# Kernel optimization log

Measured on AMD Instinct MI355X. Metric: run time of the kernel, lower is better.

Reference implementation:

```python
import jax, jax.numpy as jnp
import numpy as np

B, S, E, H, VP, L, T = 256, 256, 1024, 1024, 8, 64, 16


def setup_inputs() -> dict:
    key = jax.random.key(0)
    ks = jax.random.split(key, 10)
    image = jax.random.normal(ks[0], (B, S, E), jnp.float32)
    view_position = jax.random.uniform(ks[1], (B, VP), jnp.float32)
    label = (jax.random.uniform(ks[2], (B, T + 1, L)) > 0.5).astype(jnp.float32)
    # lengths sorted descending (length_sorted_rnn decorator), max forced to T+1
    length = jnp.sort(jax.random.randint(ks[3], (B,), 2, T + 2))[::-1]
    length = length.at[0].set(T + 1)
    def lin(k, out_d, in_d):
        return jax.random.normal(k, (out_d, in_d), jnp.float32) * (1.0 / np.sqrt(in_d)).astype(np.float32)
    IN = E + VP + 1 + L  # 1097: lstm_sizes = [embedding, view_position, 1, label]
    FC_OUT = L + H + 1 + 1  # 1090: fc_sizes = [label, hidden, 1, 1]
    return {
        'image': image, 'view_position': view_position, 'label': label, 'length': length,
        'W_h': lin(ks[4], H, E), 'b_h': jnp.zeros((H,), jnp.float32),
        'W_m': lin(ks[5], H, E), 'b_m': jnp.zeros((H,), jnp.float32),
        'W_ih': lin(ks[6], 4 * H, IN), 'W_hh': lin(ks[7], 4 * H, H),
        'b_ih': jnp.zeros((4 * H,), jnp.float32), 'b_hh': jnp.zeros((4 * H,), jnp.float32),
        'W_fc': lin(ks[8], FC_OUT, H), 'b_fc': jnp.zeros((FC_OUT,), jnp.float32),
    }


def reference(image, view_position, label, length, W_h, b_h, W_m, b_m,
              W_ih, W_hh, b_ih, b_hh, W_fc, b_fc):
    # Dropout is identity (inference). image: (B,S,E)
    image_mean = image.mean(axis=1)                      # (B,E)
    h0 = jnp.tanh(image_mean @ W_h.T + b_h)              # (B,H)
    m0 = jnp.tanh(image_mean @ W_m.T + b_m)              # (B,H)
    n_steps = label.shape[1] - 1
    bsz = image_mean.shape[0]

    def step(carry, inp):
        h, m = carry
        lab_t, t = inp
        begin = jnp.where(t == 0, 1.0, 0.0) * jnp.ones((bsz, 1), image_mean.dtype)
        x = jnp.concatenate([image_mean, view_position, begin, lab_t], axis=1)  # (B, 1097)
        gates = x @ W_ih.T + b_ih + h @ W_hh.T + b_hh    # (B, 4H)
        i, f, g, o = jnp.split(gates, 4, axis=1)
        m2 = jax.nn.sigmoid(f) * m + jax.nn.sigmoid(i) * jnp.tanh(g)
        h2 = jax.nn.sigmoid(o) * jnp.tanh(m2)
        out = h2 @ W_fc.T + b_fc                         # (B, L+H+2)
        topic = jax.nn.relu(out[:, L:L + H])
        stop = jax.nn.sigmoid(out[:, L + H:L + H + 1])
        temp = jnp.exp(out[:, L + H + 1:])
        return (h2, m2), jnp.concatenate([topic, stop, temp], axis=1)

    labels_tm = jnp.swapaxes(label[:, :n_steps], 0, 1)   # (T,B,L) time-major
    _, outs = jax.lax.scan(step, (h0, m0), (labels_tm, jnp.arange(n_steps)))
    # pad_sequence semantics: entries with t >= length-1 are zero padding
    mask = (jnp.arange(n_steps)[:, None] < (length - 1)[None, :]).astype(outs.dtype)
    return outs * mask[:, :, None]                       # (T, B, H+2) = [topic|stop|temp]
```

## Files before the change

kernel.cpp:

```cpp
#include <hip/hip_runtime.h>
#include <stdint.h>

typedef unsigned short u16;
typedef __attribute__((ext_vector_type(8))) short v8s;
typedef __attribute__((ext_vector_type(4))) float v4f;

__device__ __forceinline__ u16 f2bf(float f) {
  uint32_t x = __float_as_uint(f);
  return (u16)((x + 0x7fffu + ((x >> 16) & 1u)) >> 16);
}
__device__ __forceinline__ float bf2f(u16 u) {
  return __uint_as_float(((uint32_t)u) << 16);
}
__device__ __forceinline__ float sigf(float x) { return 1.f / (1.f + __expf(-x)); }

__device__ __forceinline__ v4f mfma16(v8s a, v8s b, v4f c) {
  return __builtin_amdgcn_mfma_f32_16x16x32_bf16(a, b, c, 0, 0, 0);
}

__device__ __forceinline__ void gll16(const u16* src, u16* ldsdst) {
  __builtin_amdgcn_global_load_lds(
      reinterpret_cast<__attribute__((address_space(1))) uint32_t*>(
          reinterpret_cast<uintptr_t>(src)),
      reinterpret_cast<__attribute__((address_space(3))) uint32_t*>(
          reinterpret_cast<uintptr_t>(ldsdst)),
      16, 0, 0);
}

__device__ __forceinline__ size_t fpoff(int row, int k, int KT) {
  return ((size_t)(((row >> 4) * KT + (k >> 6)) * 2 + ((k >> 5) & 1)) * 64 +
          ((k >> 3) & 3) * 16 + (row & 15)) * 8 + (k & 7);
}

__device__ __forceinline__ void load8(const float* p, float* f) {
  float4 a = *(const float4*)p;
  float4 b = *(const float4*)(p + 4);
  f[0]=a.x; f[1]=a.y; f[2]=a.z; f[3]=a.w; f[4]=b.x; f[5]=b.y; f[6]=b.z; f[7]=b.w;
}
__device__ __forceinline__ void store8bf(u16* dst, const float* f) {
  u16 t[8];
#pragma unroll
  for (int i = 0; i < 8; ++i) t[i] = f2bf(f[i]);
  *(v8s*)dst = *(const v8s*)t;
}

__global__ __launch_bounds__(256) void k_convert_mean(
    const float* __restrict__ Wh, const float* __restrict__ Wm,
    const float* __restrict__ Wih, const float* __restrict__ Whh,
    const float* __restrict__ Wfc, const float* __restrict__ label,
    const float* __restrict__ image,
    u16* __restrict__ wcomb, u16* __restrict__ whhb, u16* __restrict__ wfcb,
    u16* __restrict__ wlabb, u16* __restrict__ labb,
    float4* __restrict__ pacc, unsigned* __restrict__ ctr) {
  const int bid = blockIdx.x, tid = threadIdx.x;
  if (bid >= 8000) {
    ctr[(bid - 8000) * 256 + tid] = 0u;
    return;
  }
  if (bid >= 5952) {
    int bi = bid - 5952;
    int b = bi >> 3, oct = bi & 7;
    const float4* src =
        (const float4*)image + (size_t)b * 65536 + (size_t)oct * 32 * 256 + tid;
    float4 s = make_float4(0.f, 0.f, 0.f, 0.f);
#pragma unroll 8
    for (int ss = 0; ss < 32; ++ss) {
      float4 v = src[(size_t)ss * 256];
      s.x += v.x; s.y += v.y; s.z += v.z; s.w += v.w;
    }
    pacc[(size_t)bi * 256 + tid] = s;
    return;
  }
  int64_t u = (int64_t)bid * 256 + tid;
  float f[8];
  if (u < 786432) {
    int lu = (int)u;
    int r15 = lu & 15, q = (lu >> 4) & 3, s = (lu >> 6) & 1, tile = lu >> 7;
    int tk = tile & 15, tr = tile >> 4;
    int row = tr * 16 + r15, k = tk * 64 + s * 32 + q * 8;
    if (row < 1024) load8(Wh + (size_t)row * 1024 + k, f);
    else if (row < 2048) load8(Wm + (size_t)(row - 1024) * 1024 + k, f);
    else {
      const float* p = Wih + (size_t)(row - 2048) * 1097 + k;
#pragma unroll
      for (int i = 0; i < 8; ++i) f[i] = p[i];
    }
    store8bf(wcomb + (size_t)lu * 8, f);
  } else if (u < 1310720) {
    int lu = (int)(u - 786432);
    int r15 = lu & 15, q = (lu >> 4) & 3, s = (lu >> 6) & 1, tile = lu >> 7;
    int tk = tile & 15, tr = tile >> 4;
    int row = tr * 16 + r15, k = tk * 64 + s * 32 + q * 8;
    load8(Whh + (size_t)row * 1024 + k, f);
    store8bf(whhb + (size_t)lu * 8, f);
  } else if (u < 1458176) {
    int lu = (int)(u - 1310720);
    int r15 = lu & 15, q = (lu >> 4) & 3, s = (lu >> 6) & 1, tile = lu >> 7;
    int tk = tile & 15, tr = tile >> 4;
    int row = tr * 16 + r15, k = tk * 64 + s * 32 + q * 8;
    if (row < 1090) load8(Wfc + (size_t)row * 1024 + k, f);
    else {
#pragma unroll
      for (int i = 0; i < 8; ++i) f[i] = 0.f;
    }
    store8bf(wfcb + (size_t)lu * 8, f);
  } else if (u < 1490944) {
    int lu = (int)(u - 1458176);
    int r15 = lu & 15, q = (lu >> 4) & 3, s = (lu >> 6) & 1, tile = lu >> 7;
    int row = tile * 16 + r15, k = s * 32 + q * 8;
    const float* p = Wih + (size_t)row * 1097 + 1033 + k;
#pragma unroll
    for (int i = 0; i < 8; ++i) f[i] = p[i];
    store8bf(wlabb + (size_t)lu * 8, f);
  } else {
    int lu = (int)(u - 1490944);
    int r15 = lu & 15, q = (lu >> 4) & 3, s = (lu >> 6) & 1, tile = lu >> 7;
    int row = tile * 16 + r15, k = s * 32 + q * 8;
    int t = row >> 8, b = row & 255;
    load8(label + ((size_t)b * 17 + t) * 64 + k, f);
    store8bf(labb + (size_t)lu * 8, f);
  }
}

__global__ __launch_bounds__(256) void k_mean2(const float4* __restrict__ pacc,
                                               u16* __restrict__ meanbf) {
  int b = blockIdx.x, tid = threadIdx.x;
  float4 s = make_float4(0.f, 0.f, 0.f, 0.f);
#pragma unroll
  for (int q = 0; q < 8; ++q) {
    float4 v = pacc[((size_t)b * 8 + q) * 256 + tid];
    s.x += v.x; s.y += v.y; s.z += v.z; s.w += v.w;
  }
  const float inv = 1.f / 256.f;
  int k = tid * 4;
  ushort4 o;
  o.x = f2bf(s.x * inv); o.y = f2bf(s.y * inv);
  o.z = f2bf(s.z * inv); o.w = f2bf(s.w * inv);
  *(ushort4*)&meanbf[fpoff(b, k, 16)] = o;
}

__global__ __launch_bounds__(256) void k_gemm_init(
    const u16* __restrict__ meanbf, const u16* __restrict__ wcomb,
    const float* __restrict__ bh, const float* __restrict__ bm,
    const float* __restrict__ bih, const float* __restrict__ bhh,
    const float* __restrict__ vp, const float* __restrict__ Wih,
    u16* __restrict__ hbuf, float* __restrict__ mbuf, float* __restrict__ basebuf) {
  __shared__ alignas(16) u16 lA[4 * 1024];
  __shared__ alignas(16) u16 lB[4 * 1024];
  const int tid = threadIdx.x, lane = tid & 63, wid = tid >> 6;
  const int bm0 = (blockIdx.x & 3) * 64;
  const int bn0 = (blockIdx.x >> 2) * 64;
  const int wr = wid >> 1, wc = wid & 1;
  v4f acc[2][2];
#pragma unroll
  for (int i = 0; i < 2; ++i)
#pragma unroll
    for (int j = 0; j < 2; ++j) acc[i][j] = (v4f){0.f, 0.f, 0.f, 0.f};

  for (int kt = 0; kt < 16; ++kt) {
    const u16* asrc = meanbf + ((size_t)((bm0 >> 4) + wid) * 16 + kt) * 1024 + lane * 8;
    gll16(asrc, lA + wid * 1024);
    gll16(asrc + 512, lA + wid * 1024 + 512);
    const u16* bsrc = wcomb + ((size_t)((bn0 >> 4) + wid) * 16 + kt) * 1024 + lane * 8;
    gll16(bsrc, lB + wid * 1024);
    gll16(bsrc + 512, lB + wid * 1024 + 512);
    __syncthreads();
#pragma unroll
    for (int s = 0; s < 2; ++s) {
      v8s a0 = *(const v8s*)&lA[(size_t)(wr * 2) * 1024 + s * 512 + lane * 8];
      v8s a1 = *(const v8s*)&lA[(size_t)(wr * 2 + 1) * 1024 + s * 512 + lane * 8];
      v8s b0 = *(const v8s*)&lB[(size_t)(wc * 2) * 1024 + s * 512 + lane * 8];
      v8s b1 = *(const v8s*)&lB[(size_t)(wc * 2 + 1) * 1024 + s * 512 + lane * 8];
      acc[0][0] = mfma16(a0, b0, acc[0][0]);
      acc[0][1] = mfma16(a0, b1, acc[0][1]);
      acc[1][0] = mfma16(a1, b0, acc[1][0]);
      acc[1][1] = mfma16(a1, b1, acc[1][1]);
    }
    __syncthreads();
  }
#pragma unroll
  for (int fm = 0; fm < 2; ++fm)
#pragma unroll
    for (int fn = 0; fn < 2; ++fn)
#pragma unroll
      for (int rg = 0; rg < 4; ++rg) {
        int row = bm0 + wr * 32 + fm * 16 + ((lane >> 4) << 2) + rg;
        int col = bn0 + wc * 32 + fn * 16 + (lane & 15);
        float v = acc[fm][fn][rg];
        if (col < 1024) {
          hbuf[fpoff(row, col, 16)] = f2bf(tanhf(v + bh[col]));
        } else if (col < 2048) {
          int nn = col - 1024;
          mbuf[(size_t)row * 1024 + nn] = tanhf(v + bm[nn]);
        } else {
          int j = col - 2048;
          float sv = v + bih[j] + bhh[j];
#pragma unroll
          for (int q = 0; q < 8; ++q)
            sv += vp[row * 8 + q] * Wih[(size_t)j * 1097 + 1024 + q];
          basebuf[(size_t)row * 4096 + j] = sv;
        }
      }
}

__global__ __launch_bounds__(256) void k_basefull(
    const u16* __restrict__ labb, const u16* __restrict__ wlabb,
    const float* __restrict__ basebuf, const float* __restrict__ Wih,
    u16* __restrict__ bfull) {
  __shared__ alignas(16) u16 lA[4 * 1024];
  __shared__ alignas(16) u16 lB[4 * 1024];
  const int tid = threadIdx.x, lane = tid & 63, wid = tid >> 6;
  const int bm0 = (blockIdx.x & 63) * 64;
  const int bn0 = (blockIdx.x >> 6) * 64;
  const int wr = wid >> 1, wc = wid & 1;
  v4f acc[2][2];
#pragma unroll
  for (int i = 0; i < 2; ++i)
#pragma unroll
    for (int j = 0; j < 2; ++j) acc[i][j] = (v4f){0.f, 0.f, 0.f, 0.f};

  const u16* asrc = labb + (size_t)((bm0 >> 4) + wid) * 1024 + lane * 8;
  gll16(asrc, lA + wid * 1024);
  gll16(asrc + 512, lA + wid * 1024 + 512);
  const u16* bsrc = wlabb + (size_t)((bn0 >> 4) + wid) * 1024 + lane * 8;
  gll16(bsrc, lB + wid * 1024);
  gll16(bsrc + 512, lB + wid * 1024 + 512);
  __syncthreads();
#pragma unroll
  for (int s = 0; s < 2; ++s) {
    v8s a0 = *(const v8s*)&lA[(size_t)(wr * 2) * 1024 + s * 512 + lane * 8];
    v8s a1 = *(const v8s*)&lA[(size_t)(wr * 2 + 1) * 1024 + s * 512 + lane * 8];
    v8s b0 = *(const v8s*)&lB[(size_t)(wc * 2) * 1024 + s * 512 + lane * 8];
    v8s b1 = *(const v8s*)&lB[(size_t)(wc * 2 + 1) * 1024 + s * 512 + lane * 8];
    acc[0][0] = mfma16(a0, b0, acc[0][0]);
    acc[0][1] = mfma16(a0, b1, acc[0][1]);
    acc[1][0] = mfma16(a1, b0, acc[1][0]);
    acc[1][1] = mfma16(a1, b1, acc[1][1]);
  }
#pragma unroll
  for (int fm = 0; fm < 2; ++fm)
#pragma unroll
    for (int fn = 0; fn < 2; ++fn)
#pragma unroll
      for (int rg = 0; rg < 4; ++rg) {
        int r = bm0 + wr * 32 + fm * 16 + ((lane >> 4) << 2) + rg;
        int j = bn0 + wc * 32 + fn * 16 + (lane & 15);
        int t = r >> 8, b = r & 255;
        float v = acc[fm][fn][rg] + basebuf[(size_t)b * 4096 + j];
        if (t == 0) v += Wih[(size_t)j * 1097 + 1032];
        bfull[(size_t)r * 4096 + j] = f2bf(v);
      }
}

__global__ __launch_bounds__(256, 1) void k_steps(
    const u16* __restrict__ whhb, const u16* __restrict__ bfull,
    const float* __restrict__ mbuf, u16* __restrict__ hbuf,
    unsigned* __restrict__ ctr) {
  __shared__ alignas(16) u16 lA[64 * 512];
  __shared__ alignas(16) u16 lBias[8 * 512];
  __shared__ alignas(16) float lact[4][32 * 33];
  const int tid = threadIdx.x, lane = tid & 63, wid = tid >> 6;
  const int blk = blockIdx.x;
  const int n0idx = (blk & 7) * 4 + (blk >> 6);
  const int n0 = n0idx * 32;
  const int grp = (blk >> 3) & 7;
  const int b0 = grp * 32;
  const int atr = b0 >> 4;

  const int tr0 = wid * 64 + (n0 >> 4);
  v8s breg[16][2][2];
#pragma unroll
  for (int kt = 0; kt < 16; ++kt)
#pragma unroll
    for (int s = 0; s < 2; ++s)
#pragma unroll
      for (int j = 0; j < 2; ++j)
        breg[kt][s][j] =
            *(const v8s*)&whhb[((size_t)(tr0 + j) * 16 + kt) * 1024 + s * 512 + lane * 8];

  const int rowm = tid >> 3;
  const int nql = (tid & 7) * 4;
  const int b = b0 + rowm;
  const int n = n0 + nql;
  float4 mreg = *(const float4*)&mbuf[(size_t)b * 1024 + n];

  for (int t = 0; t < 16; ++t) {
    if (t > 0) {
      const unsigned* f = &ctr[((t - 1) * 8 + grp) * 32];
      for (int it = 0; it < (1 << 18); ++it) {
        unsigned v = __hip_atomic_load(&f[lane & 31], __ATOMIC_RELAXED,
                                       __HIP_MEMORY_SCOPE_AGENT);
        if (__ballot(v == 0u) == 0ull) break;
        __builtin_amdgcn_s_sleep(1);
      }
    }
    const u16* hsrc = hbuf + (size_t)t * 262144;
    __builtin_amdgcn_sched_barrier(0);
#pragma unroll
    for (int j = 0; j < 8; ++j) {
      const int hc = wid * 8 + j;
      const int i = hc >> 4, kt = (hc >> 1) & 7, s = hc & 1;
      gll16(hsrc + ((size_t)(atr + i) * 16 + kt) * 1024 + s * 512 + lane * 8,
            lA + (i * 32 + kt * 2 + s) * 512);
    }
    __builtin_amdgcn_sched_barrier(0);
#pragma unroll
    for (int j = 0; j < 8; ++j) {
      const int hc = wid * 8 + j;
      const int i = hc >> 4, kt = ((hc >> 1) & 7) + 8, s = hc & 1;
      gll16(hsrc + ((size_t)(atr + i) * 16 + kt) * 1024 + s * 512 + lane * 8,
            lA + (i * 32 + kt * 2 + s) * 512);
    }
    __builtin_amdgcn_sched_barrier(0);
#pragma unroll
    for (int c2 = 0; c2 < 2; ++c2) {
      const u16* bsrc = bfull + (size_t)t * 1048576 +
                        (size_t)(b0 + c2 * 16 + (lane >> 2)) * 4096 +
                        wid * 1024 + n0 + (lane & 3) * 8;
      gll16(bsrc, lBias + (wid * 2 + c2) * 512);
    }
    __builtin_amdgcn_sched_barrier(0);
    asm volatile("s_waitcnt vmcnt(10)" ::: "memory");
    __builtin_amdgcn_sched_barrier(0);
    __builtin_amdgcn_s_barrier();
    __builtin_amdgcn_sched_barrier(0);

    v4f acc[2][2];
#pragma unroll
    for (int i = 0; i < 2; ++i)
#pragma unroll
      for (int j = 0; j < 2; ++j) acc[i][j] = (v4f){0.f, 0.f, 0.f, 0.f};
#pragma unroll
    for (int kt = 0; kt < 8; ++kt)
#pragma unroll
      for (int s = 0; s < 2; ++s) {
        v8s a0 = *(const v8s*)&lA[(size_t)((0 * 16 + kt) * 2 + s) * 512 + lane * 8];
        v8s a1 = *(const v8s*)&lA[(size_t)((1 * 16 + kt) * 2 + s) * 512 + lane * 8];
        acc[0][0] = mfma16(a0, breg[kt][s][0], acc[0][0]);
        acc[0][1] = mfma16(a0, breg[kt][s][1], acc[0][1]);
        acc[1][0] = mfma16(a1, breg[kt][s][0], acc[1][0]);
        acc[1][1] = mfma16(a1, breg[kt][s][1], acc[1][1]);
      }

    __builtin_amdgcn_sched_barrier(0);
    asm volatile("s_waitcnt vmcnt(2)" ::: "memory");
    __builtin_amdgcn_sched_barrier(0);
    __builtin_amdgcn_s_barrier();
    __builtin_amdgcn_sched_barrier(0);
#pragma unroll
    for (int kt = 8; kt < 16; ++kt)
#pragma unroll
      for (int s = 0; s < 2; ++s) {
        v8s a0 = *(const v8s*)&lA[(size_t)((0 * 16 + kt) * 2 + s) * 512 + lane * 8];
        v8s a1 = *(const v8s*)&lA[(size_t)((1 * 16 + kt) * 2 + s) * 512 + lane * 8];
        acc[0][0] = mfma16(a0, breg[kt][s][0], acc[0][0]);
        acc[0][1] = mfma16(a0, breg[kt][s][1], acc[0][1]);
        acc[1][0] = mfma16(a1, breg[kt][s][0], acc[1][0]);
        acc[1][1] = mfma16(a1, breg[kt][s][1], acc[1][1]);
      }

#pragma unroll
    for (int fm = 0; fm < 2; ++fm)
#pragma unroll
      for (int fn = 0; fn < 2; ++fn)
#pragma unroll
        for (int rg = 0; rg < 4; ++rg) {
          int rr = fm * 16 + ((lane >> 4) << 2) + rg;
          int cc = fn * 16 + (lane & 15);
          lact[wid][rr * 33 + cc] = acc[fm][fn][rg];
        }
    __syncthreads();

    const int bofs = ((rowm & 15) * 4 + (nql >> 3)) * 8 + (nql & 7);
    const int bch = (rowm >> 4) * 512;
    float m2a[4];
    u16 h2a[4];
#pragma unroll
    for (int q = 0; q < 4; ++q) {
      float gi = lact[0][rowm * 33 + nql + q] + bf2f(lBias[0 * 1024 + bch + bofs + q]);
      float gf = lact[1][rowm * 33 + nql + q] + bf2f(lBias[1 * 1024 + bch + bofs + q]);
      float gg = lact[2][rowm * 33 + nql + q] + bf2f(lBias[2 * 1024 + bch + bofs + q]);
      float go = lact[3][rowm * 33 + nql + q] + bf2f(lBias[3 * 1024 + bch + bofs + q]);
      float mov = ((const float*)&mreg)[q];
      float m2 = sigf(gf) * mov + sigf(gi) * tanhf(gg);
      float h2 = sigf(go) * tanhf(m2);
      m2a[q] = m2;
      h2a[q] = f2bf(h2);
    }
    mreg = make_float4(m2a[0], m2a[1], m2a[2], m2a[3]);
    ushort4 ho;
    ho.x = h2a[0]; ho.y = h2a[1]; ho.z = h2a[2]; ho.w = h2a[3];
    unsigned long long hv;
    __builtin_memcpy(&hv, &ho, 8);
    __hip_atomic_store(
        reinterpret_cast<unsigned long long*>(
            &hbuf[(size_t)(t + 1) * 262144 + fpoff(b, n, 16)]),
        hv, __ATOMIC_RELAXED, __HIP_MEMORY_SCOPE_AGENT);

    if (t < 15) {
      __syncthreads();
      if (tid == 0)
        __hip_atomic_store(&ctr[(t * 8 + grp) * 32 + n0idx], 1u,
                           __ATOMIC_RELAXED, __HIP_MEMORY_SCOPE_AGENT);
    }
  }
}

__global__ __launch_bounds__(256) void k_fc(
    const u16* __restrict__ hall, const u16* __restrict__ wfcb,
    const float* __restrict__ bfc, const int* __restrict__ length,
    float* __restrict__ out) {
  __shared__ alignas(16) u16 lA[4 * 1024];
  __shared__ alignas(16) u16 lB[4 * 1024];
  const int tid = threadIdx.x, lane = tid & 63, wid = tid >> 6;
  const int bm0 = (int)(blockIdx.x % 64) * 64;
  const int bn0 = (int)(blockIdx.x / 64) * 64;
  const int wr = wid >> 1, wc = wid & 1;
  v4f acc[2][2];
#pragma unroll
  for (int i = 0; i < 2; ++i)
#pragma unroll
    for (int j = 0; j < 2; ++j) acc[i][j] = (v4f){0.f, 0.f, 0.f, 0.f};

  for (int kt = 0; kt < 16; ++kt) {
    const u16* asrc = hall + ((size_t)((bm0 >> 4) + wid) * 16 + kt) * 1024 + lane * 8;
    gll16(asrc, lA + wid * 1024);
    gll16(asrc + 512, lA + wid * 1024 + 512);
    const u16* bsrc = wfcb + ((size_t)((bn0 >> 4) + wid) * 16 + kt) * 1024 + lane * 8;
    gll16(bsrc, lB + wid * 1024);
    gll16(bsrc + 512, lB + wid * 1024 + 512);
    __syncthreads();
#pragma unroll
    for (int s = 0; s < 2; ++s) {
      v8s a0 = *(const v8s*)&lA[(size_t)(wr * 2) * 1024 + s * 512 + lane * 8];
      v8s a1 = *(const v8s*)&lA[(size_t)(wr * 2 + 1) * 1024 + s * 512 + lane * 8];
      v8s b0 = *(const v8s*)&lB[(size_t)(wc * 2) * 1024 + s * 512 + lane * 8];
      v8s b1 = *(const v8s*)&lB[(size_t)(wc * 2 + 1) * 1024 + s * 512 + lane * 8];
      acc[0][0] = mfma16(a0, b0, acc[0][0]);
      acc[0][1] = mfma16(a0, b1, acc[0][1]);
      acc[1][0] = mfma16(a1, b0, acc[1][0]);
      acc[1][1] = mfma16(a1, b1, acc[1][1]);
    }
    __syncthreads();
  }
#pragma unroll
  for (int fm = 0; fm < 2; ++fm)
#pragma unroll
    for (int fn = 0; fn < 2; ++fn)
#pragma unroll
      for (int rg = 0; rg < 4; ++rg) {
        int r = bm0 + wr * 32 + fm * 16 + ((lane >> 4) << 2) + rg;
        int j = bn0 + wc * 32 + fn * 16 + (lane & 15);
        if (j < 64 || j >= 1090) continue;
        int t = r >> 8, b = r & 255;
        float v = acc[fm][fn][rg] + bfc[j];
        int c;
        if (j < 1088) { c = j - 64; v = fmaxf(v, 0.f); }
        else if (j == 1088) { c = 1024; v = 1.f / (1.f + expf(-v)); }
        else { c = 1025; v = expf(v); }
        if (t >= length[b] - 1) v = 0.f;
        out[((size_t)t * 256 + b) * 1026 + c] = v;
      }
}

extern "C" void kernel_launch(void* const* d_in, const int* in_sizes, int n_in,
                              void* d_out, int out_size, void* d_ws, size_t ws_size,
                              hipStream_t stream) {
  (void)in_sizes; (void)n_in; (void)out_size; (void)ws_size;
  const float* image  = (const float*)d_in[0];
  const float* vp     = (const float*)d_in[1];
  const float* label  = (const float*)d_in[2];
  const int*   length = (const int*)d_in[3];
  const float* Wh  = (const float*)d_in[4];
  const float* bh  = (const float*)d_in[5];
  const float* Wm  = (const float*)d_in[6];
  const float* bm  = (const float*)d_in[7];
  const float* Wih = (const float*)d_in[8];
  const float* Whh = (const float*)d_in[9];
  const float* bih = (const float*)d_in[10];
  const float* bhh = (const float*)d_in[11];
  const float* Wfc = (const float*)d_in[12];
  const float* bfc = (const float*)d_in[13];
  float* out = (float*)d_out;
  char* ws = (char*)d_ws;

  size_t off = 0;
  u16* wcomb  = (u16*)(ws + off); off += (size_t)6144 * 1024 * 2;
  u16* whhb   = (u16*)(ws + off); off += (size_t)4096 * 1024 * 2;
  u16* wfcb   = (u16*)(ws + off); off += (size_t)1152 * 1024 * 2;
  u16* wlabb  = (u16*)(ws + off); off += (size_t)4096 * 64 * 2;
  u16* labb   = (u16*)(ws + off); off += (size_t)4096 * 64 * 2;
  u16* meanbf = (u16*)(ws + off); off += (size_t)256 * 1024 * 2;
  u16* hbuf   = (u16*)(ws + off); off += (size_t)17 * 256 * 1024 * 2;
  float* mbuf    = (float*)(ws + off); off += (size_t)256 * 1024 * 4;
  float* basebuf = (float*)(ws + off); off += (size_t)256 * 4096 * 4;
  u16* bfull  = (u16*)(ws + off); off += (size_t)16 * 256 * 4096 * 2;
  unsigned* ctr = (unsigned*)(ws + off); off += 4096 * 4;
  float4* pacc = (float4*)bfull;

  k_convert_mean<<<8016, 256, 0, stream>>>(Wh, Wm, Wih, Whh, Wfc, label, image,
                                           wcomb, whhb, wfcb, wlabb, labb, pacc, ctr);
  k_mean2<<<256, 256, 0, stream>>>(pacc, meanbf);
  k_gemm_init<<<384, 256, 0, stream>>>(meanbf, wcomb, bh, bm, bih, bhh, vp, Wih,
                                       hbuf, mbuf, basebuf);
  k_basefull<<<4096, 256, 0, stream>>>(labb, wlabb, basebuf, Wih, bfull);
  k_steps<<<256, 256, 0, stream>>>(whhb, bfull, mbuf, hbuf, ctr);
  k_fc<<<1152, 256, 0, stream>>>(hbuf + (size_t)256 * 1024, wfcb, bfc, length, out);
}
```

Before: 225.6 us.

## Fuse label-projection GEMM into recurrent step kernel, drop bfull precompute

Removes the separate k_basefull kernel, which materialised a 16x256x4096 bf16 bias tensor. The recurrent kernel now loads the label tiles into LDS once and keeps the label weights and base biases in registers. Each step adds the label contribution with four extra MFMAs per wave. This saves one launch and a large global write and read, but adds LDS use (64 KB more), register pressure in a kernel limited to one block per CU, and compute on the serial critical path.

```diff
diff --git a/kernel.cpp b/kernel.cpp
--- a/kernel.cpp
+++ b/kernel.cpp
@@ -203,61 +203,13 @@
       }
 }
 
-__global__ __launch_bounds__(256) void k_basefull(
-    const u16* __restrict__ labb, const u16* __restrict__ wlabb,
-    const float* __restrict__ basebuf, const float* __restrict__ Wih,
-    u16* __restrict__ bfull) {
-  __shared__ alignas(16) u16 lA[4 * 1024];
-  __shared__ alignas(16) u16 lB[4 * 1024];
-  const int tid = threadIdx.x, lane = tid & 63, wid = tid >> 6;
-  const int bm0 = (blockIdx.x & 63) * 64;
-  const int bn0 = (blockIdx.x >> 6) * 64;
-  const int wr = wid >> 1, wc = wid & 1;
-  v4f acc[2][2];
-#pragma unroll
-  for (int i = 0; i < 2; ++i)
-#pragma unroll
-    for (int j = 0; j < 2; ++j) acc[i][j] = (v4f){0.f, 0.f, 0.f, 0.f};
-
-  const u16* asrc = labb + (size_t)((bm0 >> 4) + wid) * 1024 + lane * 8;
-  gll16(asrc, lA + wid * 1024);
-  gll16(asrc + 512, lA + wid * 1024 + 512);
-  const u16* bsrc = wlabb + (size_t)((bn0 >> 4) + wid) * 1024 + lane * 8;
-  gll16(bsrc, lB + wid * 1024);
-  gll16(bsrc + 512, lB + wid * 1024 + 512);
-  __syncthreads();
-#pragma unroll
-  for (int s = 0; s < 2; ++s) {
-    v8s a0 = *(const v8s*)&lA[(size_t)(wr * 2) * 1024 + s * 512 + lane * 8];
-    v8s a1 = *(const v8s*)&lA[(size_t)(wr * 2 + 1) * 1024 + s * 512 + lane * 8];
-    v8s b0 = *(const v8s*)&lB[(size_t)(wc * 2) * 1024 + s * 512 + lane * 8];
-    v8s b1 = *(const v8s*)&lB[(size_t)(wc * 2 + 1) * 1024 + s * 512 + lane * 8];
-    acc[0][0] = mfma16(a0, b0, acc[0][0]);
-    acc[0][1] = mfma16(a0, b1, acc[0][1]);
-    acc[1][0] = mfma16(a1, b0, acc[1][0]);
-    acc[1][1] = mfma16(a1, b1, acc[1][1]);
-  }
-#pragma unroll
-  for (int fm = 0; fm < 2; ++fm)
-#pragma unroll
-    for (int fn = 0; fn < 2; ++fn)
-#pragma unroll
-      for (int rg = 0; rg < 4; ++rg) {
-        int r = bm0 + wr * 32 + fm * 16 + ((lane >> 4) << 2) + rg;
-        int j = bn0 + wc * 32 + fn * 16 + (lane & 15);
-        int t = r >> 8, b = r & 255;
-        float v = acc[fm][fn][rg] + basebuf[(size_t)b * 4096 + j];
-        if (t == 0) v += Wih[(size_t)j * 1097 + 1032];
-        bfull[(size_t)r * 4096 + j] = f2bf(v);
-      }
-}
-
 __global__ __launch_bounds__(256, 1) void k_steps(
-    const u16* __restrict__ whhb, const u16* __restrict__ bfull,
-    const float* __restrict__ mbuf, u16* __restrict__ hbuf,
-    unsigned* __restrict__ ctr) {
+    const u16* __restrict__ whhb, const u16* __restrict__ wlabb,
+    const u16* __restrict__ labb, const float* __restrict__ basebuf,
+    const float* __restrict__ Wih, const float* __restrict__ mbuf,
+    u16* __restrict__ hbuf, unsigned* __restrict__ ctr) {
   __shared__ alignas(16) u16 lA[64 * 512];
-  __shared__ alignas(16) u16 lBias[8 * 512];
+  __shared__ alignas(16) u16 lLab[64 * 512];
   __shared__ alignas(16) float lact[4][32 * 33];
   const int tid = threadIdx.x, lane = tid & 63, wid = tid >> 6;
   const int blk = blockIdx.x;
@@ -267,6 +219,14 @@
   const int b0 = grp * 32;
   const int atr = b0 >> 4;
 
+#pragma unroll
+  for (int j = 0; j < 16; ++j) {
+    const int c = wid * 16 + j;
+    const int t = c >> 2, i = (c >> 1) & 1, s = c & 1;
+    gll16(labb + (size_t)(t * 16 + atr + i) * 1024 + s * 512 + lane * 8,
+          lLab + c * 512);
+  }
+
   const int tr0 = wid * 64 + (n0 >> 4);
   v8s breg[16][2][2];
 #pragma unroll
@@ -277,12 +237,27 @@
       for (int j = 0; j < 2; ++j)
         breg[kt][s][j] =
             *(const v8s*)&whhb[((size_t)(tr0 + j) * 16 + kt) * 1024 + s * 512 + lane * 8];
+  v8s wlreg[2][2];
+#pragma unroll
+  for (int s = 0; s < 2; ++s)
+#pragma unroll
+    for (int j = 0; j < 2; ++j)
+      wlreg[s][j] = *(const v8s*)&wlabb[(size_t)(tr0 + j) * 1024 + s * 512 + lane * 8];
 
   const int rowm = tid >> 3;
   const int nql = (tid & 7) * 4;
   const int b = b0 + rowm;
   const int n = n0 + nql;
   float4 mreg = *(const float4*)&mbuf[(size_t)b * 1024 + n];
+  float4 bse[4], wbv[4];
+#pragma unroll
+  for (int g = 0; g < 4; ++g) {
+    bse[g] = *(const float4*)&basebuf[(size_t)b * 4096 + g * 1024 + n];
+#pragma unroll
+    for (int q = 0; q < 4; ++q)
+      ((float*)&wbv[g])[q] = Wih[(size_t)(g * 1024 + n + q) * 1097 + 1032];
+  }
+  __syncthreads();
 
   for (int t = 0; t < 16; ++t) {
     if (t > 0) {
@@ -312,24 +287,27 @@
             lA + (i * 32 + kt * 2 + s) * 512);
     }
     __builtin_amdgcn_sched_barrier(0);
-#pragma unroll
-    for (int c2 = 0; c2 < 2; ++c2) {
-      const u16* bsrc = bfull + (size_t)t * 1048576 +
-                        (size_t)(b0 + c2 * 16 + (lane >> 2)) * 4096 +
-                        wid * 1024 + n0 + (lane & 3) * 8;
-      gll16(bsrc, lBias + (wid * 2 + c2) * 512);
-    }
-    __builtin_amdgcn_sched_barrier(0);
-    asm volatile("s_waitcnt vmcnt(10)" ::: "memory");
+
+    v4f acc[2][2];
+#pragma unroll
+    for (int i = 0; i < 2; ++i)
+#pragma unroll
+      for (int j = 0; j < 2; ++j) acc[i][j] = (v4f){0.f, 0.f, 0.f, 0.f};
+#pragma unroll
+    for (int s = 0; s < 2; ++s) {
+      v8s aL0 = *(const v8s*)&lLab[(size_t)(t * 4 + 0 * 2 + s) * 512 + lane * 8];
+      v8s aL1 = *(const v8s*)&lLab[(size_t)(t * 4 + 1 * 2 + s) * 512 + lane * 8];
+      acc[0][0] = mfma16(aL0, wlreg[s][0], acc[0][0]);
+      acc[0][1] = mfma16(aL0, wlreg[s][1], acc[0][1]);
+      acc[1][0] = mfma16(aL1, wlreg[s][0], acc[1][0]);
+      acc[1][1] = mfma16(aL1, wlreg[s][1], acc[1][1]);
+    }
+
+    __builtin_amdgcn_sched_barrier(0);
+    asm volatile("s_waitcnt vmcnt(8)" ::: "memory");
     __builtin_amdgcn_sched_barrier(0);
     __builtin_amdgcn_s_barrier();
     __builtin_amdgcn_sched_barrier(0);
-
-    v4f acc[2][2];
-#pragma unroll
-    for (int i = 0; i < 2; ++i)
-#pragma unroll
-      for (int j = 0; j < 2; ++j) acc[i][j] = (v4f){0.f, 0.f, 0.f, 0.f};
 #pragma unroll
     for (int kt = 0; kt < 8; ++kt)
 #pragma unroll
@@ -343,7 +321,7 @@
       }
 
     __builtin_amdgcn_sched_barrier(0);
-    asm volatile("s_waitcnt vmcnt(2)" ::: "memory");
+    asm volatile("s_waitcnt vmcnt(0)" ::: "memory");
     __builtin_amdgcn_sched_barrier(0);
     __builtin_amdgcn_s_barrier();
     __builtin_amdgcn_sched_barrier(0);
@@ -371,16 +349,18 @@
         }
     __syncthreads();
 
-    const int bofs = ((rowm & 15) * 4 + (nql >> 3)) * 8 + (nql & 7);
-    const int bch = (rowm >> 4) * 512;
     float m2a[4];
     u16 h2a[4];
 #pragma unroll
     for (int q = 0; q < 4; ++q) {
-      float gi = lact[0][rowm * 33 + nql + q] + bf2f(lBias[0 * 1024 + bch + bofs + q]);
-      float gf = lact[1][rowm * 33 + nql + q] + bf2f(lBias[1 * 1024 + bch + bofs + q]);
-      float gg = lact[2][rowm * 33 + nql + q] + bf2f(lBias[2 * 1024 + bch + bofs + q]);
-      float go = lact[3][rowm * 33 + nql + q] + bf2f(lBias[3 * 1024 + bch + bofs + q]);
+      float b0q = ((const float*)&bse[0])[q] + (t == 0 ? ((const float*)&wbv[0])[q] : 0.f);
+      float b1q = ((const float*)&bse[1])[q] + (t == 0 ? ((const float*)&wbv[1])[q] : 0.f);
+      float b2q = ((const float*)&bse[2])[q] + (t == 0 ? ((const float*)&wbv[2])[q] : 0.f);
+      float b3q = ((const float*)&bse[3])[q] + (t == 0 ? ((const float*)&wbv[3])[q] : 0.f);
+      float gi = lact[0][rowm * 33 + nql + q] + b0q;
+      float gf = lact[1][rowm * 33 + nql + q] + b1q;
+      float gg = lact[2][rowm * 33 + nql + q] + b2q;
+      float go = lact[3][rowm * 33 + nql + q] + b3q;
       float mov = ((const float*)&mreg)[q];
       float m2 = sigf(gf) * mov + sigf(gi) * tanhf(gg);
       float h2 = sigf(go) * tanhf(m2);
@@ -494,16 +474,14 @@
   u16* hbuf   = (u16*)(ws + off); off += (size_t)17 * 256 * 1024 * 2;
   float* mbuf    = (float*)(ws + off); off += (size_t)256 * 1024 * 4;
   float* basebuf = (float*)(ws + off); off += (size_t)256 * 4096 * 4;
-  u16* bfull  = (u16*)(ws + off); off += (size_t)16 * 256 * 4096 * 2;
   unsigned* ctr = (unsigned*)(ws + off); off += 4096 * 4;
-  float4* pacc = (float4*)bfull;
+  float4* pacc = (float4*)(ws + off); off += (size_t)2048 * 256 * 16;
 
   k_convert_mean<<<8016, 256, 0, stream>>>(Wh, Wm, Wih, Whh, Wfc, label, image,
                                            wcomb, whhb, wfcb, wlabb, labb, pacc, ctr);
   k_mean2<<<256, 256, 0, stream>>>(pacc, meanbf);
   k_gemm_init<<<384, 256, 0, stream>>>(meanbf, wcomb, bh, bm, bih, bhh, vp, Wih,
                                        hbuf, mbuf, basebuf);
-  k_basefull<<<4096, 256, 0, stream>>>(labb, wlabb, basebuf, Wih, bfull);
-  k_steps<<<256, 256, 0, stream>>>(whhb, bfull, mbuf, hbuf, ctr);
+  k_steps<<<256, 256, 0, stream>>>(whhb, wlabb, labb, basebuf, Wih, mbuf, hbuf, ctr);
   k_fc<<<1152, 256, 0, stream>>>(hbuf + (size_t)256 * 1024, wfcb, bfc, length, out);
 }
```

After: 197.5 us. 12.5% less time.
